# Kernel tuning notes

Hardware: AMD Instinct MI355X
Metric: run time of the kernel (lower is better)

The kernel has to match this reference:

```python
import jax, jax.numpy as jnp
import numpy as np

N, E, IN, H, C, G = 50000, 1600000, 128, 4, 32, 64  # nodes, edges, in_ch, heads, hidden, graphs
OUT = 1
NEG_SLOPE = 0.2


def setup_inputs() -> dict:
    key = jax.random.key(0)
    ks = jax.random.split(key, 16)
    d = {
        "x": jax.random.normal(ks[0], (N, IN), dtype=jnp.float32),
        "edge_index": jax.random.randint(ks[1], (2, E), 0, N, dtype=jnp.int64),
        "batch": jnp.sort(jax.random.randint(ks[2], (N,), 0, G, dtype=jnp.int64)),
    }
    s = 1.0 / np.sqrt(IN)
    # layer 0: in=IN, layer 1: in=H*C (=128)
    d["W0"] = jax.random.normal(ks[3], (IN, H * C), dtype=jnp.float32) * s
    d["a_src0"] = jax.random.normal(ks[4], (H, C), dtype=jnp.float32) * s
    d["a_dst0"] = jax.random.normal(ks[5], (H, C), dtype=jnp.float32) * s
    d["b0"] = jnp.zeros((H * C,), dtype=jnp.float32)
    d["W1"] = jax.random.normal(ks[6], (H * C, H * C), dtype=jnp.float32) * s
    d["a_src1"] = jax.random.normal(ks[7], (H, C), dtype=jnp.float32) * s
    d["a_dst1"] = jax.random.normal(ks[8], (H, C), dtype=jnp.float32) * s
    d["b1"] = jnp.zeros((H * C,), dtype=jnp.float32)
    d["lin_w"] = jax.random.normal(ks[9], (H * C, OUT), dtype=jnp.float32) * s
    d["lin_b"] = jnp.zeros((OUT,), dtype=jnp.float32)
    return d


def gat_conv(x, src, dst, W, a_src, a_dst, b):
    # x: [N, F_in]; src/dst: [E'] (self-loops already appended, PyG default)
    n = x.shape[0]
    xw = (x @ W).reshape(n, H, C)                      # [N, H, C]
    alpha_s = jnp.sum(xw * a_src, axis=-1)             # [N, H]
    alpha_d = jnp.sum(xw * a_dst, axis=-1)             # [N, H]
    e = jax.nn.leaky_relu(alpha_s[src] + alpha_d[dst], NEG_SLOPE)  # [E', H]
    # segment softmax over edges grouped by destination node
    m = jax.ops.segment_max(e, dst, num_segments=n)    # [N, H]
    ex = jnp.exp(e - m[dst])
    denom = jax.ops.segment_sum(ex, dst, num_segments=n)
    alpha = ex / denom[dst]                            # [E', H]
    msg = xw[src] * alpha[:, :, None]                  # [E', H, C]
    out = jax.ops.segment_sum(msg, dst, num_segments=n)
    return out.reshape(n, H * C) + b


def reference(x, edge_index, batch, W0, a_src0, a_dst0, b0, W1, a_src1, a_dst1, b1, lin_w, lin_b):
    loop = jnp.arange(N, dtype=edge_index.dtype)
    src = jnp.concatenate([edge_index[0], loop])
    dst = jnp.concatenate([edge_index[1], loop])
    h = gat_conv(x.astype(jnp.float32), src, dst, W0, a_src0, a_dst0, b0)
    h = jax.nn.elu(h)  # dropout is identity in eval mode
    h = gat_conv(h, src, dst, W1, a_src1, a_dst1, b1)
    h = jax.nn.elu(h)
    # global_mean_pool
    sums = jax.ops.segment_sum(h, batch, num_segments=G)          # [G, H*C]
    cnts = jax.ops.segment_sum(jnp.ones((N,), h.dtype), batch, num_segments=G)
    pooled = sums / jnp.maximum(cnts, 1.0)[:, None]
    return (pooled @ lin_w + lin_b).squeeze()                     # [G]
```

## Files before the change

### kernel.cpp

```cpp
#include <hip/hip_runtime.h>
#include <hip/hip_bf16.h>

#define NN 50000
#define EE 1600000
#define NEDGE (EE + NN)
#define HH 4
#define HC 128
#define GG 64
#define GMT 64
#define GMT2 32
#define NBKT 196
#define BCAP 12544
#define BKE 2048
#define NB1 ((EE + BKE - 1) / BKE)
#define GB ((NN + GMT - 1) / GMT)

__device__ __forceinline__ float lrelu(float x) { return fmaxf(x, 0.2f * x); }

__device__ __forceinline__ unsigned packbf2(float a, float b) {
    unsigned ua = __float_as_uint(a);
    ua = (ua + 0x7fffu + ((ua >> 16) & 1u)) >> 16;
    unsigned ub = __float_as_uint(b);
    ub = (ub + 0x7fffu + ((ub >> 16) & 1u)) >> 16;
    return ua | (ub << 16);
}

__global__ __launch_bounds__(256) void binit(int* __restrict__ bcur) {
    int t = blockIdx.x * 256 + threadIdx.x;
    if (t < NBKT) bcur[t] = t * BCAP;
}

__global__ __launch_bounds__(256) void g0bkt(
    const float* __restrict__ X, const float* __restrict__ W,
    const float* __restrict__ a_src, const float* __restrict__ a_dst,
    unsigned* __restrict__ xwb, float* __restrict__ as_, float* __restrict__ ad_,
    const int* __restrict__ ei, int* __restrict__ bcur, unsigned* __restrict__ pairs) {
    __shared__ union U {
        float xs[GMT2][HC + 4];
        struct {
            int cnt[NBKT], off[NBKT], gbase[NBKT];
            int wsum[4], woff[4];
            unsigned stage[BKE];
        } b;
    } u;
    int t = threadIdx.x;
    int id = (int)(blockIdx.x / 3);
    int type = (int)(blockIdx.x % 3);

    if (type < 2) {
        int n0 = (id * 2 + type) * GMT2;
        for (int i = t; i < GMT2 * (HC / 4); i += 256) {
            int r = i >> 5, c4 = i & 31;
            int n = n0 + r;
            float4 v = (n < NN) ? ((const float4*)X)[(size_t)n * 32 + c4]
                                : make_float4(0.f, 0.f, 0.f, 0.f);
            *(float4*)&u.xs[r][c4 * 4] = v;
        }
        __syncthreads();
        int jg = t & 31;
        int ng = t >> 5;
        float4 acc[4] = {};
        for (int k = 0; k < HC; k += 4) {
            float4 wr[4];
#pragma unroll
            for (int dk = 0; dk < 4; ++dk) wr[dk] = ((const float4*)W)[(k + dk) * 32 + jg];
#pragma unroll
            for (int r = 0; r < 4; ++r) {
                float4 xv = *(const float4*)&u.xs[ng * 4 + r][k];
                acc[r].x = fmaf(xv.x, wr[0].x, acc[r].x);
                acc[r].y = fmaf(xv.x, wr[0].y, acc[r].y);
                acc[r].z = fmaf(xv.x, wr[0].z, acc[r].z);
                acc[r].w = fmaf(xv.x, wr[0].w, acc[r].w);
                acc[r].x = fmaf(xv.y, wr[1].x, acc[r].x);
                acc[r].y = fmaf(xv.y, wr[1].y, acc[r].y);
                acc[r].z = fmaf(xv.y, wr[1].z, acc[r].z);
                acc[r].w = fmaf(xv.y, wr[1].w, acc[r].w);
                acc[r].x = fmaf(xv.z, wr[2].x, acc[r].x);
                acc[r].y = fmaf(xv.z, wr[2].y, acc[r].y);
                acc[r].z = fmaf(xv.z, wr[2].z, acc[r].z);
                acc[r].w = fmaf(xv.z, wr[2].w, acc[r].w);
                acc[r].x = fmaf(xv.w, wr[3].x, acc[r].x);
                acc[r].y = fmaf(xv.w, wr[3].y, acc[r].y);
                acc[r].z = fmaf(xv.w, wr[3].z, acc[r].z);
                acc[r].w = fmaf(xv.w, wr[3].w, acc[r].w);
            }
        }
        float4 asv = ((const float4*)a_src)[jg];
        float4 adv = ((const float4*)a_dst)[jg];
#pragma unroll
        for (int r = 0; r < 4; ++r) {
            int n = n0 + ng * 4 + r;
            float ps = acc[r].x * asv.x + acc[r].y * asv.y + acc[r].z * asv.z + acc[r].w * asv.w;
            float pd = acc[r].x * adv.x + acc[r].y * adv.y + acc[r].z * adv.z + acc[r].w * adv.w;
            ps += __shfl_xor(ps, 1); pd += __shfl_xor(pd, 1);
            ps += __shfl_xor(ps, 2); pd += __shfl_xor(pd, 2);
            ps += __shfl_xor(ps, 4); pd += __shfl_xor(pd, 4);
            if (n < NN) {
                ((uint2*)xwb)[(size_t)n * 32 + jg] =
                    make_uint2(packbf2(acc[r].x, acc[r].y), packbf2(acc[r].z, acc[r].w));
                if ((jg & 7) == 0) {
                    int h = jg >> 3;
                    as_[n * HH + h] = ps;
                    ad_[n * HH + h] = pd;
                }
            }
        }
    } else {
        int e0 = id * BKE;
        int n = EE - e0; if (n > BKE) n = BKE;
        for (int i = t; i < NBKT; i += 256) u.b.cnt[i] = 0;
        __syncthreads();
        unsigned dv[8], sv[8];
        int rk[8];
#pragma unroll
        for (int k = 0; k < 8; ++k) {
            int i = t + k * 256;
            if (i < n) {
                dv[k] = (unsigned)ei[EE + e0 + i];
                sv[k] = (unsigned)ei[e0 + i];
                rk[k] = atomicAdd(&u.b.cnt[dv[k] >> 8], 1);
            }
        }
        __syncthreads();
        {
            int v = (t < NBKT) ? u.b.cnt[t] : 0;
            int lane = t & 63, wv = t >> 6;
            int x = v;
#pragma unroll
            for (int o = 1; o < 64; o <<= 1) { int y = __shfl_up(x, o); if (lane >= o) x += y; }
            if (lane == 63) u.b.wsum[wv] = x;
            __syncthreads();
            if (t == 0) { int r = 0; for (int k2 = 0; k2 < 4; ++k2) { u.b.woff[k2] = r; r += u.b.wsum[k2]; } }
            __syncthreads();
            if (t < NBKT) u.b.off[t] = x - v + u.b.woff[wv];
        }
        __syncthreads();
#pragma unroll
        for (int k = 0; k < 8; ++k) {
            int i = t + k * 256;
            if (i < n) u.b.stage[u.b.off[dv[k] >> 8] + rk[k]] = (dv[k] << 16) | sv[k];
        }
        __syncthreads();
        if (t < NBKT) { int c = u.b.cnt[t]; u.b.gbase[t] = c ? atomicAdd(&bcur[t], c) : 0; }
        __syncthreads();
        for (int i = t; i < n; i += 256) {
            unsigned pr = u.b.stage[i];
            int b = (int)(pr >> 24);
            pairs[(size_t)u.b.gbase[b] + (i - u.b.off[b])] = pr;
        }
    }
}

__global__ __launch_bounds__(512) void debucket(const unsigned* __restrict__ pairs,
                                                const int* __restrict__ bcur,
                                                int* __restrict__ row_start,
                                                int* __restrict__ esrc) {
    __shared__ int cnt[256], off[256], cur[256];
    __shared__ int wsum[4], woff[4];
    __shared__ int wred[8];
    __shared__ int stage[BCAP + 256];
    int b = blockIdx.x, t = threadIdx.x;
    int n0 = b * 256;
    int nnode = NN - n0; if (nnode > 256) nnode = 256;
    int pcnt = bcur[b] - b * BCAP;

    int base;
    {
        int v = 0;
        if (t < b) {
            int pc = bcur[t] - t * BCAP;
            int nd = (t < NBKT - 1) ? 256 : (NN - (NBKT - 1) * 256);
            v = pc + nd;
        }
        int lane = t & 63, wv = t >> 6;
#pragma unroll
        for (int o = 1; o < 64; o <<= 1) v += __shfl_xor(v, o);
        if (lane == 0) wred[wv] = v;
        __syncthreads();
        if (t == 0) { int s = 0; for (int k = 0; k < 8; ++k) s += wred[k]; wred[0] = s; }
        __syncthreads();
        base = wred[0];
    }
    __syncthreads();
    if (t < 256) cnt[t] = 0;
    __syncthreads();
    for (int i = t; i < pcnt; i += 512)
        atomicAdd(&cnt[(pairs[(size_t)b * BCAP + i] >> 16) & 255u], 1);
    __syncthreads();
    {
        int v = 0, x = 0;
        int lane = t & 63, wv = t >> 6;
        if (t < 256) {
            v = cnt[t] + (t < nnode ? 1 : 0);
            x = v;
#pragma unroll
            for (int o = 1; o < 64; o <<= 1) { int y = __shfl_up(x, o); if (lane >= o) x += y; }
            if (lane == 63) wsum[wv] = x;
        }
        __syncthreads();
        if (t == 0) { int r = 0; for (int k = 0; k < 4; ++k) { woff[k] = r; r += wsum[k]; } }
        __syncthreads();
        if (t < 256) off[t] = x - v + woff[wv];
    }
    __syncthreads();
    if (t < nnode) {
        int o = off[t];
        stage[o] = n0 + t;
        cur[t] = o + 1;
        row_start[n0 + t] = base + o;
    }
    __syncthreads();
    for (int i = t; i < pcnt; i += 512) {
        unsigned pr = pairs[(size_t)b * BCAP + i];
        int p = atomicAdd(&cur[(pr >> 16) & 255u], 1);
        stage[p] = (int)(pr & 0xFFFFu);
    }
    __syncthreads();
    int tot = pcnt + nnode;
    for (int i = t; i < tot; i += 512) esrc[base + i] = stage[i];
    if (b == NBKT - 1 && t == 0) row_start[NN] = NEDGE;
}

__global__ __launch_bounds__(256) void gemm_alpha(
    const float* __restrict__ X, const float* __restrict__ W,
    const float* __restrict__ a_src, const float* __restrict__ a_dst,
    unsigned* __restrict__ xwb, float* __restrict__ as_, float* __restrict__ ad_) {
    __shared__ float xs[GMT][HC + 4];
    int tid = threadIdx.x;
    int n0 = blockIdx.x * GMT;
    for (int i = tid; i < GMT * (HC / 4); i += 256) {
        int r = i >> 5, c4 = i & 31;
        int n = n0 + r;
        float4 v = (n < NN) ? ((const float4*)X)[(size_t)n * 32 + c4]
                            : make_float4(0.f, 0.f, 0.f, 0.f);
        *(float4*)&xs[r][c4 * 4] = v;
    }
    __syncthreads();

    int jg = tid & 31;
    int ng = tid >> 5;
    float4 acc[8] = {};
    for (int k = 0; k < HC; k += 4) {
        float4 wr[4];
#pragma unroll
        for (int dk = 0; dk < 4; ++dk) wr[dk] = ((const float4*)W)[(k + dk) * 32 + jg];
#pragma unroll
        for (int r = 0; r < 8; ++r) {
            float4 xv = *(const float4*)&xs[ng * 8 + r][k];
            acc[r].x = fmaf(xv.x, wr[0].x, acc[r].x);
            acc[r].y = fmaf(xv.x, wr[0].y, acc[r].y);
            acc[r].z = fmaf(xv.x, wr[0].z, acc[r].z);
            acc[r].w = fmaf(xv.x, wr[0].w, acc[r].w);
            acc[r].x = fmaf(xv.y, wr[1].x, acc[r].x);
            acc[r].y = fmaf(xv.y, wr[1].y, acc[r].y);
            acc[r].z = fmaf(xv.y, wr[1].z, acc[r].z);
            acc[r].w = fmaf(xv.y, wr[1].w, acc[r].w);
            acc[r].x = fmaf(xv.z, wr[2].x, acc[r].x);
            acc[r].y = fmaf(xv.z, wr[2].y, acc[r].y);
            acc[r].z = fmaf(xv.z, wr[2].z, acc[r].z);
            acc[r].w = fmaf(xv.z, wr[2].w, acc[r].w);
            acc[r].x = fmaf(xv.w, wr[3].x, acc[r].x);
            acc[r].y = fmaf(xv.w, wr[3].y, acc[r].y);
            acc[r].z = fmaf(xv.w, wr[3].z, acc[r].z);
            acc[r].w = fmaf(xv.w, wr[3].w, acc[r].w);
        }
    }
    float4 asv = ((const float4*)a_src)[jg];
    float4 adv = ((const float4*)a_dst)[jg];
#pragma unroll
    for (int r = 0; r < 8; ++r) {
        int n = n0 + ng * 8 + r;
        float ps = acc[r].x * asv.x + acc[r].y * asv.y + acc[r].z * asv.z + acc[r].w * asv.w;
        float pd = acc[r].x * adv.x + acc[r].y * adv.y + acc[r].z * adv.z + acc[r].w * adv.w;
        ps += __shfl_xor(ps, 1); pd += __shfl_xor(pd, 1);
        ps += __shfl_xor(ps, 2); pd += __shfl_xor(pd, 2);
        ps += __shfl_xor(ps, 4); pd += __shfl_xor(pd, 4);
        if (n < NN) {
            ((uint2*)xwb)[(size_t)n * 32 + jg] =
                make_uint2(packbf2(acc[r].x, acc[r].y), packbf2(acc[r].z, acc[r].w));
            if ((jg & 7) == 0) {
                int h = jg >> 3;
                as_[n * HH + h] = ps;
                ad_[n * HH + h] = pd;
            }
        }
    }
}

#define SWSTR 66
__global__ __launch_bounds__(256) void aggregate(
    const int* __restrict__ esrc, const int* __restrict__ row_start,
    const float* __restrict__ as_, const float* __restrict__ ad_,
    const unsigned* __restrict__ xwb, const float* __restrict__ bias,
    float* __restrict__ out) {
    __shared__ float2 sw_all[4][4 * SWSTR];
    int wid = (int)(threadIdx.x >> 6);
    int node = blockIdx.x * 4 + wid;
    if (node >= NN) return;
    int lane = threadIdx.x & 63;
    float2* sw = &sw_all[wid][0];
    int beg = row_start[node];
    int end = row_start[node + 1];
    float4 ad = ((const float4*)ad_)[node];

    int sub = lane >> 4;
    int c8 = lane & 15;
    int h = c8 >> 2;
    const char* xwp = (const char*)xwb + (c8 << 4);
    const char* asp = (const char*)as_;
    float4 accA = make_float4(0.f, 0.f, 0.f, 0.f);
    float4 accB = make_float4(0.f, 0.f, 0.f, 0.f);
    float dloc = 0.f;

    for (int base = beg; base < end; base += 64) {
        int i = base + lane;
        int cnt = end - base; if (cnt > 64) cnt = 64;
        if (i < end) {
            int s = esrc[i];
            float4 av = *(const float4*)(asp + ((unsigned)s << 4));
            float w0 = __expf(lrelu(av.x + ad.x));
            float w1 = __expf(lrelu(av.y + ad.y));
            float w2 = __expf(lrelu(av.z + ad.z));
            float w3 = __expf(lrelu(av.w + ad.w));
            float sf = __int_as_float(s);
            sw[0 * SWSTR + lane] = make_float2(sf, w0);
            sw[1 * SWSTR + lane] = make_float2(sf, w1);
            sw[2 * SWSTR + lane] = make_float2(sf, w2);
            sw[3 * SWSTR + lane] = make_float2(sf, w3);
        }
        int iters = (cnt + 3) >> 2;
        bool ok = sub < cnt;
        float2 sv = sw[h * SWSTR + (ok ? sub : 0)];
        float wj = ok ? sv.y : 0.f;
        unsigned row = ok ? ((unsigned)__float_as_int(sv.x) << 8) : 0u;
        uint4 v = *(const uint4*)(xwp + row);
        for (int it = 1; it <= iters; ++it) {
            int j1 = (it << 2) + sub;
            bool ok1 = j1 < cnt;
            float2 sv1 = sw[h * SWSTR + (ok1 ? j1 : 0)];
            float w1 = ok1 ? sv1.y : 0.f;
            unsigned row1 = ok1 ? ((unsigned)__float_as_int(sv1.x) << 8) : 0u;
            uint4 v1 = *(const uint4*)(xwp + row1);
            dloc += wj;
            accA.x = fmaf(wj, __uint_as_float(v.x << 16), accA.x);
            accA.y = fmaf(wj, __uint_as_float(v.x & 0xffff0000u), accA.y);
            accA.z = fmaf(wj, __uint_as_float(v.y << 16), accA.z);
            accA.w = fmaf(wj, __uint_as_float(v.y & 0xffff0000u), accA.w);
            accB.x = fmaf(wj, __uint_as_float(v.z << 16), accB.x);
            accB.y = fmaf(wj, __uint_as_float(v.z & 0xffff0000u), accB.y);
            accB.z = fmaf(wj, __uint_as_float(v.w << 16), accB.z);
            accB.w = fmaf(wj, __uint_as_float(v.w & 0xffff0000u), accB.w);
            v = v1; wj = w1;
        }
    }
#pragma unroll
    for (int off = 16; off <= 32; off <<= 1) {
        accA.x += __shfl_xor(accA.x, off);
        accA.y += __shfl_xor(accA.y, off);
        accA.z += __shfl_xor(accA.z, off);
        accA.w += __shfl_xor(accA.w, off);
        accB.x += __shfl_xor(accB.x, off);
        accB.y += __shfl_xor(accB.y, off);
        accB.z += __shfl_xor(accB.z, off);
        accB.w += __shfl_xor(accB.w, off);
        dloc += __shfl_xor(dloc, off);
    }
    if (sub == 0) {
        float inv = 1.f / dloc;
        float4 bb0 = ((const float4*)bias)[c8 * 2];
        float4 bb1 = ((const float4*)bias)[c8 * 2 + 1];
        float4 oA, oB;
        oA.x = fmaf(accA.x, inv, bb0.x);
        oA.y = fmaf(accA.y, inv, bb0.y);
        oA.z = fmaf(accA.z, inv, bb0.z);
        oA.w = fmaf(accA.w, inv, bb0.w);
        oB.x = fmaf(accB.x, inv, bb1.x);
        oB.y = fmaf(accB.y, inv, bb1.y);
        oB.z = fmaf(accB.z, inv, bb1.z);
        oB.w = fmaf(accB.w, inv, bb1.w);
        oA.x = oA.x > 0.f ? oA.x : expm1f(oA.x);
        oA.y = oA.y > 0.f ? oA.y : expm1f(oA.y);
        oA.z = oA.z > 0.f ? oA.z : expm1f(oA.z);
        oA.w = oA.w > 0.f ? oA.w : expm1f(oA.w);
        oB.x = oB.x > 0.f ? oB.x : expm1f(oB.x);
        oB.y = oB.y > 0.f ? oB.y : expm1f(oB.y);
        oB.z = oB.z > 0.f ? oB.z : expm1f(oB.z);
        oB.w = oB.w > 0.f ? oB.w : expm1f(oB.w);
        ((float4*)out)[(size_t)node * 32 + c8 * 2] = oA;
        ((float4*)out)[(size_t)node * 32 + c8 * 2 + 1] = oB;
    }
}

__global__ __launch_bounds__(128) void pool(
    const float* __restrict__ h1, const int* __restrict__ batch,
    float* __restrict__ sums, float* __restrict__ cnts) {
    int j = threadIdx.x;
    int n0 = blockIdx.x * 64;
    int n1 = n0 + 64; if (n1 > NN) n1 = NN;
    if (n0 >= NN) return;
    int cur = batch[n0];
    float local = 0.f;
    int cnt = 0;
    for (int n = n0; n < n1; ++n) {
        int g = batch[n];
        if (g != cur) {
            atomicAdd(&sums[cur * HC + j], local);
            if (j == 0) atomicAdd(&cnts[cur], (float)cnt);
            local = 0.f; cnt = 0; cur = g;
        }
        local += h1[(size_t)n * HC + j];
        ++cnt;
    }
    atomicAdd(&sums[cur * HC + j], local);
    if (j == 0) atomicAdd(&cnts[cur], (float)cnt);
}

__global__ __launch_bounds__(128) void head_out(
    const float* __restrict__ sums, const float* __restrict__ cnts,
    const float* __restrict__ lin_w, const float* __restrict__ lin_b,
    float* __restrict__ out) {
    int g = blockIdx.x;
    int j = threadIdx.x;
    float c = cnts[g];
    c = c > 1.f ? c : 1.f;
    float v = sums[g * HC + j] / c * lin_w[j];
    __shared__ float red[HC];
    red[j] = v;
    __syncthreads();
    for (int off = 64; off > 0; off >>= 1) {
        if (j < off) red[j] += red[j + off];
        __syncthreads();
    }
    if (j == 0) out[g] = red[0] + lin_b[0];
}

extern "C" void kernel_launch(void* const* d_in, const int* in_sizes, int n_in,
                              void* d_out, int out_size, void* d_ws, size_t ws_size,
                              hipStream_t stream) {
    const float* x   = (const float*)d_in[0];
    const int*   ei  = (const int*)d_in[1];
    const int*   bat = (const int*)d_in[2];
    const float* W0  = (const float*)d_in[3];
    const float* as0 = (const float*)d_in[4];
    const float* ad0 = (const float*)d_in[5];
    const float* b0  = (const float*)d_in[6];
    const float* W1  = (const float*)d_in[7];
    const float* as1 = (const float*)d_in[8];
    const float* ad1 = (const float*)d_in[9];
    const float* b1  = (const float*)d_in[10];
    const float* lw  = (const float*)d_in[11];
    const float* lb  = (const float*)d_in[12];
    float* out = (float*)d_out;

    char* w = (char*)d_ws;
    unsigned* xwb = (unsigned*)w; w += (size_t)NN * HC * 2;
    float* h0  = (float*)w;  w += (size_t)NN * HC * 4;
    float* as_ = (float*)w;  w += (size_t)NN * HH * 4;
    float* ad_ = (float*)w;  w += (size_t)NN * HH * 4;
    int* row_start = (int*)w; w += (size_t)(NN + 1) * 4;
    int* bcur      = (int*)w; w += (size_t)NBKT * 4;
    int* esrc      = (int*)w; w += (size_t)NEDGE * 4;
    unsigned* pairs = (unsigned*)w; w += (size_t)NBKT * BCAP * 4;
    float* sums = (float*)w; w += (size_t)GG * HC * 4;
    float* cnts = (float*)w; w += (size_t)GG * 4;

    const int ab = (NN + 3) / 4;

    binit<<<1, 256, 0, stream>>>(bcur);
    g0bkt<<<NB1 * 3, 256, 0, stream>>>(x, W0, as0, ad0, xwb, as_, ad_,
                                       ei, bcur, pairs);
    debucket<<<NBKT, 512, 0, stream>>>(pairs, bcur, row_start, esrc);

    aggregate<<<ab, 256, 0, stream>>>(esrc, row_start, as_, ad_, xwb, b0, h0);

    gemm_alpha<<<GB, 256, 0, stream>>>(h0, W1, as1, ad1, xwb, as_, ad_);
    aggregate<<<ab, 256, 0, stream>>>(esrc, row_start, as_, ad_, xwb, b1, h0);

    hipMemsetAsync(sums, 0, ((size_t)GG * HC + GG) * 4, stream);
    pool<<<(NN + 63) / 64, 128, 0, stream>>>(h0, bat, sums, cnts);
    head_out<<<GG, 128, 0, stream>>>(sums, cnts, lw, lb, out);
}
```

Baseline: 247.4 us.

## Fuse global mean pooling into second GAT aggregate via per-node atomics

The second aggregate launch now adds each node's ELU output straight into per-graph sums and counts with float atomics, instead of writing h1 out and running a separate pool kernel. This removes the pool launch and the write and reread of the full node-feature tensor, and moves the sums memset to the start of the stream. The cost is about 128 atomics per node, contending on only 64×128 addresses because batch is sorted. That is far more atomic traffic than the old per-block partial sums and may serialize in L2. Float summation order also changes.

Result: slower. 762.3 us (+208.1%).

```diff
diff --git a/kernel.cpp b/kernel.cpp
--- a/kernel.cpp
+++ b/kernel.cpp
@@ -292,7 +292,9 @@
     const int* __restrict__ esrc, const int* __restrict__ row_start,
     const float* __restrict__ as_, const float* __restrict__ ad_,
     const unsigned* __restrict__ xwb, const float* __restrict__ bias,
-    float* __restrict__ out) {
+    float* __restrict__ out,
+    const int* __restrict__ batch, float* __restrict__ sums,
+    float* __restrict__ cnts, int do_pool) {
     __shared__ float2 sw_all[4][4 * SWSTR];
     int wid = (int)(threadIdx.x >> 6);
     int node = blockIdx.x * 4 + wid;
@@ -386,33 +388,23 @@
         oB.y = oB.y > 0.f ? oB.y : expm1f(oB.y);
         oB.z = oB.z > 0.f ? oB.z : expm1f(oB.z);
         oB.w = oB.w > 0.f ? oB.w : expm1f(oB.w);
-        ((float4*)out)[(size_t)node * 32 + c8 * 2] = oA;
-        ((float4*)out)[(size_t)node * 32 + c8 * 2 + 1] = oB;
-    }
-}
-
-__global__ __launch_bounds__(128) void pool(
-    const float* __restrict__ h1, const int* __restrict__ batch,
-    float* __restrict__ sums, float* __restrict__ cnts) {
-    int j = threadIdx.x;
-    int n0 = blockIdx.x * 64;
-    int n1 = n0 + 64; if (n1 > NN) n1 = NN;
-    if (n0 >= NN) return;
-    int cur = batch[n0];
-    float local = 0.f;
-    int cnt = 0;
-    for (int n = n0; n < n1; ++n) {
-        int g = batch[n];
-        if (g != cur) {
-            atomicAdd(&sums[cur * HC + j], local);
-            if (j == 0) atomicAdd(&cnts[cur], (float)cnt);
-            local = 0.f; cnt = 0; cur = g;
-        }
-        local += h1[(size_t)n * HC + j];
-        ++cnt;
-    }
-    atomicAdd(&sums[cur * HC + j], local);
-    if (j == 0) atomicAdd(&cnts[cur], (float)cnt);
+        if (do_pool) {
+            int g = batch[node];
+            float* sg = sums + (size_t)g * HC + c8 * 8;
+            atomicAdd(sg + 0, oA.x);
+            atomicAdd(sg + 1, oA.y);
+            atomicAdd(sg + 2, oA.z);
+            atomicAdd(sg + 3, oA.w);
+            atomicAdd(sg + 4, oB.x);
+            atomicAdd(sg + 5, oB.y);
+            atomicAdd(sg + 6, oB.z);
+            atomicAdd(sg + 7, oB.w);
+            if (c8 == 0) atomicAdd(&cnts[g], 1.0f);
+        } else {
+            ((float4*)out)[(size_t)node * 32 + c8 * 2] = oA;
+            ((float4*)out)[(size_t)node * 32 + c8 * 2 + 1] = oB;
+        }
+    }
 }
 
 __global__ __launch_bounds__(128) void head_out(
@@ -466,17 +458,18 @@
 
     const int ab = (NN + 3) / 4;
 
+    hipMemsetAsync(sums, 0, ((size_t)GG * HC + GG) * 4, stream);
     binit<<<1, 256, 0, stream>>>(bcur);
     g0bkt<<<NB1 * 3, 256, 0, stream>>>(x, W0, as0, ad0, xwb, as_, ad_,
                                        ei, bcur, pairs);
     debucket<<<NBKT, 512, 0, stream>>>(pairs, bcur, row_start, esrc);
 
-    aggregate<<<ab, 256, 0, stream>>>(esrc, row_start, as_, ad_, xwb, b0, h0);
+    aggregate<<<ab, 256, 0, stream>>>(esrc, row_start, as_, ad_, xwb, b0, h0,
+                                      bat, sums, cnts, 0);
 
     gemm_alpha<<<GB, 256, 0, stream>>>(h0, W1, as1, ad1, xwb, as_, ad_);
-    aggregate<<<ab, 256, 0, stream>>>(esrc, row_start, as_, ad_, xwb, b1, h0);
-
-    hipMemsetAsync(sums, 0, ((size_t)GG * HC + GG) * 4, stream);
-    pool<<<(NN + 63) / 64, 128, 0, stream>>>(h0, bat, sums, cnts);
+    aggregate<<<ab, 256, 0, stream>>>(esrc, row_start, as_, ad_, xwb, b1, h0,
+                                      bat, sums, cnts, 1);
+
     head_out<<<GG, 128, 0, stream>>>(sums, cnts, lw, lb, out);
 }
```
